# Optimization experiments

Measured on AMD Instinct MI355X. Metric: run time of the kernel, lower is better.

The kernel has to match this reference:

```python
import jax, jax.numpy as jnp
import numpy as np

N_BLOBS = 8
# blob_configs (static, from init_kwargs)
SIDE_RIGHT = np.array([1, 0, 1, 0, 1, 0, 1, 0], dtype=bool)  # right -> positions[:, :3]
START_Y = np.array([0.1, 0.2, 0.3, 0.4, 0.5, 0.6, 0.7, 0.8], dtype=np.float32)
START_X = np.array([0.8, 0.7, 0.6, 0.5, 0.4, 0.3, 0.2, 0.1], dtype=np.float32)
START_S = np.full(N_BLOBS, 0.05, dtype=np.float32)
A_MIN = np.full(N_BLOBS, 0.5, dtype=np.float32)
A_MAX = np.full(N_BLOBS, 2.0, dtype=np.float32)
EPS = 1e-6


def setup_inputs() -> dict:
    key = jax.random.key(0)
    ks = jax.random.split(key, 8)
    B, H = 256, 64
    return {
        "positions": jax.random.normal(ks[0], (B, 6), jnp.float32),
        "W1": jax.random.normal(ks[1], (N_BLOBS, 3, H), jnp.float32) * 0.1,
        "b1": jnp.zeros((N_BLOBS, H), jnp.float32),
        "W2": jax.random.normal(ks[2], (N_BLOBS, H, H), jnp.float32) * 0.1,
        "b2": jnp.zeros((N_BLOBS, H), jnp.float32),
        "W3": jax.random.normal(ks[3], (N_BLOBS, H, 5), jnp.float32) * 0.1,
        "b3": jnp.zeros((N_BLOBS, 5), jnp.float32),
        "target_size": 256,
        "blobs_scale_factor": jnp.ones((), jnp.float32),
    }


def _encode_all(positions, W1, b1, W2, b2, W3, b3):
    """Per-blob MLP over selected half of positions -> [N_BLOBS, B, 5] blob data."""
    side = jnp.asarray(SIDE_RIGHT)[:, None, None]  # [N,1,1]
    # right blobs use first 3 coords, left blobs use last 3
    pos = jnp.where(side, positions[None, :, :3], positions[None, :, 3:]) * 100.0  # [N,B,3]
    h = jax.nn.relu(jnp.einsum('nbi,nih->nbh', pos, W1) + b1[:, None, :])
    h = jax.nn.relu(jnp.einsum('nbh,nhk->nbk', h, W2) + b2[:, None, :])
    bd = jnp.einsum('nbh,nhk->nbk', h, W3) + b3[:, None, :]  # [N,B,5]
    y = jax.nn.sigmoid(bd[..., 0]) + jnp.asarray(START_Y)[:, None]
    x = jax.nn.sigmoid(bd[..., 1]) + jnp.asarray(START_X)[:, None]
    s = bd[..., 2] + jnp.asarray(START_S)[:, None]
    a = jnp.asarray(A_MIN)[:, None] + jax.nn.sigmoid(bd[..., 3]) * (jnp.asarray(A_MAX) - jnp.asarray(A_MIN))[:, None]
    th = jax.nn.sigmoid(bd[..., 4]) * jnp.pi
    return y, x, s, a, th  # each [N,B]


def _splat(y, x, s, a, th, T):
    """Elliptical gaussian splat for one blob: params [B] -> image [B,T,T]."""
    coords = (jnp.arange(T, dtype=jnp.float32) + 0.5) / T  # pixel centers in [0,1)
    dy = coords[None, :, None] - y[:, None, None]  # [B,T,1]
    dx = coords[None, None, :] - x[:, None, None]  # [B,1,T]
    c = jnp.cos(th)[:, None, None]
    sn = jnp.sin(th)[:, None, None]
    u = c * dy + sn * dx   # rotated coords [B,T,T]
    v = -sn * dy + c * dx
    sa = (s * a)[:, None, None] + EPS   # major sigma
    sb = (s / (a + EPS))[:, None, None] + EPS  # minor sigma
    return jnp.exp(-0.5 * ((u / sa) ** 2 + (v / sb) ** 2))


def reference(positions, W1, b1, W2, b2, W3, b3, target_size, blobs_scale_factor):
    y, x, s, a, th = _encode_all(positions, W1, b1, W2, b2, W3, b3)
    s = s * blobs_scale_factor
    B = positions.shape[0]
    img = jnp.zeros((B, target_size, target_size), positions.dtype)
    for i in range(N_BLOBS):  # small fixed blob count; sequential blend as in source
        cur = _splat(y[i], x[i], s[i], a[i], th[i], target_size)
        img = img * cur + cur  # mul then add with same blob image
    return img
```

## Files before the change

### kernel.cpp

```cpp
#include <hip/hip_runtime.h>
#include <math.h>

#define NBLOBS 8
#define HID    64
#define TSZ    256
#define BATCH  256
#define EPSV   1e-6f

#if __has_builtin(__builtin_amdgcn_exp2f)
#define FAST_EXP(x) __builtin_amdgcn_exp2f(x)
#define PRESCALE 0.8493218002880191f
#else
#define FAST_EXP(x) __expf(x)
#define PRESCALE 0.7071067811865476f
#endif

__device__ __forceinline__ float sigmoidf_(float x) {
    return 1.0f / (1.0f + __expf(-x));
}

__global__ __launch_bounds__(BATCH) void encode_kernel(
    const float* __restrict__ positions,
    const float* __restrict__ W1,
    const float* __restrict__ b1,
    const float* __restrict__ W2,
    const float* __restrict__ b2,
    const float* __restrict__ W3,
    const float* __restrict__ b3,
    const float* __restrict__ scale_ptr,
    float* __restrict__ params)
{
    const int n   = blockIdx.x;
    const int tid = threadIdx.x;

    __shared__ float sW1[3 * HID];
    __shared__ float sB1[HID];
    __shared__ float sW2[HID * HID];
    __shared__ float sB2[HID];
    __shared__ float sW3[HID * 5];
    __shared__ float sB3[5];

    for (int i = tid; i < 3 * HID; i += BATCH) sW1[i] = W1[n * 3 * HID + i];
    for (int i = tid; i < HID;     i += BATCH) sB1[i] = b1[n * HID + i];
    for (int i = tid; i < HID*HID; i += BATCH) sW2[i] = W2[n * HID * HID + i];
    for (int i = tid; i < HID;     i += BATCH) sB2[i] = b2[n * HID + i];
    for (int i = tid; i < HID * 5; i += BATCH) sW3[i] = W3[n * HID * 5 + i];
    if (tid < 5) sB3[tid] = b3[n * 5 + tid];
    __syncthreads();

    const int b = tid;
    const int off = (n & 1) ? 3 : 0;
    const float p0 = positions[b * 6 + off + 0] * 100.0f;
    const float p1 = positions[b * 6 + off + 1] * 100.0f;
    const float p2 = positions[b * 6 + off + 2] * 100.0f;

    float h1[HID];
#pragma unroll
    for (int k = 0; k < HID; ++k) {
        float acc = sB1[k];
        acc = fmaf(p0, sW1[0 * HID + k], acc);
        acc = fmaf(p1, sW1[1 * HID + k], acc);
        acc = fmaf(p2, sW1[2 * HID + k], acc);
        h1[k] = fmaxf(acc, 0.0f);
    }

    float h2[HID];
#pragma unroll
    for (int k = 0; k < HID; ++k) {
        float acc = sB2[k];
#pragma unroll
        for (int h = 0; h < HID; ++h)
            acc = fmaf(h1[h], sW2[h * HID + k], acc);
        h2[k] = fmaxf(acc, 0.0f);
    }

    float bd[5];
#pragma unroll
    for (int j = 0; j < 5; ++j) {
        float acc = sB3[j];
#pragma unroll
        for (int h = 0; h < HID; ++h)
            acc = fmaf(h2[h], sW3[h * 5 + j], acc);
        bd[j] = acc;
    }

    const float scale = scale_ptr[0];
    const float y  = sigmoidf_(bd[0]) + 0.1f * (float)(n + 1);
    const float x  = sigmoidf_(bd[1]) + 0.1f * (float)(8 - n);
    const float s  = (bd[2] + 0.05f) * scale;
    const float a  = 0.5f + sigmoidf_(bd[3]) * 1.5f;
    const float th = sigmoidf_(bd[4]) * 3.14159265358979323846f;

    float sn, c;
    sincosf(th, &sn, &c);

    const float sa = s * a + EPSV;
    const float sb = s / (a + EPSV) + EPSV;
    const float ia = PRESCALE / sa;
    const float ib = PRESCALE / sb;

    float* p = params + (n * BATCH + b) * 8;
    p[0] = y;
    p[1] = x;
    p[2] = c * ia;
    p[3] = sn * ia;
    p[4] = -sn * ib;
    p[5] = c * ib;
    p[6] = 0.0f;
    p[7] = 0.0f;
}

__global__ __launch_bounds__(256) void splat_kernel(
    const float* __restrict__ params,
    float* __restrict__ out)
{
    const int b = blockIdx.y;

    __shared__ float sp[NBLOBS * 8];
    if (threadIdx.x < NBLOBS * 8) {
        const int n = threadIdx.x >> 3;
        const int f = threadIdx.x & 7;
        sp[threadIdx.x] = params[(n * BATCH + b) * 8 + f];
    }
    __syncthreads();

    const int row = blockIdx.x * 4 + (threadIdx.x >> 6);
    const int jb  = (threadIdx.x & 63) * 4;
    const float ci = ((float)row + 0.5f) * (1.0f / TSZ);

    float xv[NBLOBS], Bv[NBLOBS], Dv[NBLOBS], uA[NBLOBS], vC[NBLOBS];
#pragma unroll
    for (int n = 0; n < NBLOBS; ++n) {
        const float y = sp[n * 8 + 0];
        xv[n] = sp[n * 8 + 1];
        const float A = sp[n * 8 + 2];
        Bv[n] = sp[n * 8 + 3];
        const float C = sp[n * 8 + 4];
        Dv[n] = sp[n * 8 + 5];
        const float dy = ci - y;
        uA[n] = A * dy;
        vC[n] = C * dy;
    }

    float4 res;
    float* rp = &res.x;
#pragma unroll
    for (int jj = 0; jj < 4; ++jj) {
        const float cj = ((float)(jb + jj) + 0.5f) * (1.0f / TSZ);
        float img = 0.0f;
#pragma unroll
        for (int n = 0; n < NBLOBS; ++n) {
            const float dx = cj - xv[n];
            const float u = fmaf(Bv[n], dx, uA[n]);
            const float v = fmaf(Dv[n], dx, vC[n]);
            const float t = fmaf(-u, u, -(v * v));
            const float cur = FAST_EXP(t);
            img = fmaf(img, cur, cur);
        }
        rp[jj] = img;
    }

    float4* dst = (float4*)(out + (size_t)b * TSZ * TSZ + row * TSZ + jb);
    *dst = res;
}

extern "C" void kernel_launch(void* const* d_in, const int* in_sizes, int n_in,
                              void* d_out, int out_size, void* d_ws, size_t ws_size,
                              hipStream_t stream) {
    const float* positions = (const float*)d_in[0];
    const float* W1        = (const float*)d_in[1];
    const float* b1        = (const float*)d_in[2];
    const float* W2        = (const float*)d_in[3];
    const float* b2        = (const float*)d_in[4];
    const float* W3        = (const float*)d_in[5];
    const float* b3        = (const float*)d_in[6];
    const float* scale_ptr = (const float*)d_in[8];

    float* params = (float*)d_ws;
    float* out    = (float*)d_out;

    encode_kernel<<<dim3(NBLOBS), dim3(BATCH), 0, stream>>>(
        positions, W1, b1, W2, b2, W3, b3, scale_ptr, params);

    splat_kernel<<<dim3(TSZ / 4, BATCH), dim3(256), 0, stream>>>(params, out);
}
```

Measured before the change: 130.0 us.

## Expand gaussian exponent as quadratic in row coordinate and restructure encode MLP

The splat exponent is rewritten as a quadratic in the row coordinate, with per-blob coefficients precomputed in the encoder. Each thread now computes 8 rows of one column, so each pixel-blob pair costs two FMAs plus an exp instead of several multiplies. The encoder is split across 4 blocks per blob of 64 threads, with float4 weight loads and an outer-product loop order for the second layer. The expanded quadratic may lose precision through cancellation, and output stores become scalar, coalesced per row, instead of float4.

```diff
diff --git a/kernel.cpp b/kernel.cpp
--- a/kernel.cpp
+++ b/kernel.cpp
@@ -19,7 +19,7 @@
     return 1.0f / (1.0f + __expf(-x));
 }
 
-__global__ __launch_bounds__(BATCH) void encode_kernel(
+__global__ __launch_bounds__(64) void encode_kernel(
     const float* __restrict__ positions,
     const float* __restrict__ W1,
     const float* __restrict__ b1,
@@ -40,15 +40,21 @@
     __shared__ float sW3[HID * 5];
     __shared__ float sB3[5];
 
-    for (int i = tid; i < 3 * HID; i += BATCH) sW1[i] = W1[n * 3 * HID + i];
-    for (int i = tid; i < HID;     i += BATCH) sB1[i] = b1[n * HID + i];
-    for (int i = tid; i < HID*HID; i += BATCH) sW2[i] = W2[n * HID * HID + i];
-    for (int i = tid; i < HID;     i += BATCH) sB2[i] = b2[n * HID + i];
-    for (int i = tid; i < HID * 5; i += BATCH) sW3[i] = W3[n * HID * 5 + i];
+    for (int i = tid; i < 3 * HID; i += 64) sW1[i] = W1[n * 3 * HID + i];
+    for (int i = tid; i < HID; i += 64) {
+        sB1[i] = b1[n * HID + i];
+        sB2[i] = b2[n * HID + i];
+    }
+    {
+        float4*       s4 = (float4*)sW2;
+        const float4* g4 = (const float4*)(W2 + n * HID * HID);
+        for (int i = tid; i < HID * HID / 4; i += 64) s4[i] = g4[i];
+    }
+    for (int i = tid; i < HID * 5; i += 64) sW3[i] = W3[n * HID * 5 + i];
     if (tid < 5) sB3[tid] = b3[n * 5 + tid];
     __syncthreads();
 
-    const int b = tid;
+    const int b = blockIdx.y * 64 + tid;
     const int off = (n & 1) ? 3 : 0;
     const float p0 = positions[b * 6 + off + 0] * 100.0f;
     const float p1 = positions[b * 6 + off + 1] * 100.0f;
@@ -64,24 +70,33 @@
         h1[k] = fmaxf(acc, 0.0f);
     }
 
-    float h2[HID];
-#pragma unroll
-    for (int k = 0; k < HID; ++k) {
-        float acc = sB2[k];
-#pragma unroll
-        for (int h = 0; h < HID; ++h)
-            acc = fmaf(h1[h], sW2[h * HID + k], acc);
-        h2[k] = fmaxf(acc, 0.0f);
-    }
+    float acc[HID];
+#pragma unroll
+    for (int k = 0; k < HID; ++k) acc[k] = sB2[k];
+#pragma unroll
+    for (int h = 0; h < HID; ++h) {
+        const float xh = h1[h];
+#pragma unroll
+        for (int k4 = 0; k4 < HID / 4; ++k4) {
+            const float4 w = *(const float4*)&sW2[h * HID + 4 * k4];
+            acc[4 * k4 + 0] = fmaf(xh, w.x, acc[4 * k4 + 0]);
+            acc[4 * k4 + 1] = fmaf(xh, w.y, acc[4 * k4 + 1]);
+            acc[4 * k4 + 2] = fmaf(xh, w.z, acc[4 * k4 + 2]);
+            acc[4 * k4 + 3] = fmaf(xh, w.w, acc[4 * k4 + 3]);
+        }
+    }
+#pragma unroll
+    for (int k = 0; k < HID; ++k) acc[k] = fmaxf(acc[k], 0.0f);
 
     float bd[5];
 #pragma unroll
-    for (int j = 0; j < 5; ++j) {
-        float acc = sB3[j];
-#pragma unroll
-        for (int h = 0; h < HID; ++h)
-            acc = fmaf(h2[h], sW3[h * 5 + j], acc);
-        bd[j] = acc;
+    for (int j = 0; j < 5; ++j) bd[j] = sB3[j];
+#pragma unroll
+    for (int h = 0; h < HID; ++h) {
+        const float xh = acc[h];
+#pragma unroll
+        for (int j = 0; j < 5; ++j)
+            bd[j] = fmaf(xh, sW3[h * 5 + j], bd[j]);
     }
 
     const float scale = scale_ptr[0];
@@ -99,14 +114,23 @@
     const float ia = PRESCALE / sa;
     const float ib = PRESCALE / sb;
 
+    const float A = c * ia;
+    const float B = sn * ia;
+    const float C = -sn * ib;
+    const float D = c * ib;
+
+    const float M   = -2.0f * (A * B + C * D);
+    const float Qx  = -(B * B + D * D);
+    const float del = -(A * A + C * C);
+
     float* p = params + (n * BATCH + b) * 8;
-    p[0] = y;
-    p[1] = x;
-    p[2] = c * ia;
-    p[3] = sn * ia;
-    p[4] = -sn * ib;
-    p[5] = c * ib;
-    p[6] = 0.0f;
+    p[0] = x;
+    p[1] = M;
+    p[2] = Qx;
+    p[3] = del;
+    p[4] = -2.0f * y * del;
+    p[5] = -y;
+    p[6] = del * y * y;
     p[7] = 0.0f;
 }
 
@@ -114,7 +138,7 @@
     const float* __restrict__ params,
     float* __restrict__ out)
 {
-    const int b = blockIdx.y;
+    const int b = blockIdx.z;
 
     __shared__ float sp[NBLOBS * 8];
     if (threadIdx.x < NBLOBS * 8) {
@@ -124,44 +148,48 @@
     }
     __syncthreads();
 
-    const int row = blockIdx.x * 4 + (threadIdx.x >> 6);
-    const int jb  = (threadIdx.x & 63) * 4;
-    const float ci = ((float)row + 0.5f) * (1.0f / TSZ);
-
-    float xv[NBLOBS], Bv[NBLOBS], Dv[NBLOBS], uA[NBLOBS], vC[NBLOBS];
+    const int j  = blockIdx.x * 64 + (threadIdx.x & 63);
+    const int r0 = blockIdx.y * 32 + (threadIdx.x >> 6) * 8;
+    const float cj = ((float)j + 0.5f) * (1.0f / TSZ);
+
+    float ci[8], ci2[8];
+#pragma unroll
+    for (int r = 0; r < 8; ++r) {
+        ci[r]  = ((float)(r0 + r) + 0.5f) * (1.0f / TSZ);
+        ci2[r] = ci[r] * ci[r];
+    }
+
+    float img[8];
+#pragma unroll
+    for (int r = 0; r < 8; ++r) img[r] = 0.0f;
+
 #pragma unroll
     for (int n = 0; n < NBLOBS; ++n) {
-        const float y = sp[n * 8 + 0];
-        xv[n] = sp[n * 8 + 1];
-        const float A = sp[n * 8 + 2];
-        Bv[n] = sp[n * 8 + 3];
-        const float C = sp[n * 8 + 4];
-        Dv[n] = sp[n * 8 + 5];
-        const float dy = ci - y;
-        uA[n] = A * dy;
-        vC[n] = C * dy;
-    }
-
-    float4 res;
-    float* rp = &res.x;
-#pragma unroll
-    for (int jj = 0; jj < 4; ++jj) {
-        const float cj = ((float)(jb + jj) + 0.5f) * (1.0f / TSZ);
-        float img = 0.0f;
-#pragma unroll
-        for (int n = 0; n < NBLOBS; ++n) {
-            const float dx = cj - xv[n];
-            const float u = fmaf(Bv[n], dx, uA[n]);
-            const float v = fmaf(Dv[n], dx, vC[n]);
-            const float t = fmaf(-u, u, -(v * v));
+        const float x    = sp[n * 8 + 0];
+        const float M    = sp[n * 8 + 1];
+        const float Qx   = sp[n * 8 + 2];
+        const float del  = sp[n * 8 + 3];
+        const float m2yd = sp[n * 8 + 4];
+        const float negy = sp[n * 8 + 5];
+        const float y2d  = sp[n * 8 + 6];
+
+        const float dx  = cj - x;
+        const float dx2 = dx * dx;
+        const float e   = M * dx;
+        const float b1c = e + m2yd;
+        const float b0c = fmaf(negy, e, fmaf(Qx, dx2, y2d));
+
+#pragma unroll
+        for (int r = 0; r < 8; ++r) {
+            const float t   = fmaf(ci2[r], del, fmaf(ci[r], b1c, b0c));
             const float cur = FAST_EXP(t);
-            img = fmaf(img, cur, cur);
+            img[r] = fmaf(img[r], cur, cur);
         }
-        rp[jj] = img;
-    }
-
-    float4* dst = (float4*)(out + (size_t)b * TSZ * TSZ + row * TSZ + jb);
-    *dst = res;
+    }
+
+    float* dst = out + (size_t)b * TSZ * TSZ + (size_t)r0 * TSZ + j;
+#pragma unroll
+    for (int r = 0; r < 8; ++r) dst[r * TSZ] = img[r];
 }
 
 extern "C" void kernel_launch(void* const* d_in, const int* in_sizes, int n_in,
@@ -179,8 +207,8 @@
     float* params = (float*)d_ws;
     float* out    = (float*)d_out;
 
-    encode_kernel<<<dim3(NBLOBS), dim3(BATCH), 0, stream>>>(
+    encode_kernel<<<dim3(NBLOBS, BATCH / 64), dim3(64), 0, stream>>>(
         positions, W1, b1, W2, b2, W3, b3, scale_ptr, params);
 
-    splat_kernel<<<dim3(TSZ / 4, BATCH), dim3(256), 0, stream>>>(params, out);
-}
+    splat_kernel<<<dim3(TSZ / 64, TSZ / 32, BATCH), dim3(256), 0, stream>>>(params, out);
+}
```

Result: no change. 127.7 us (-1.8%).
